# Kernel optimization log

Measured on AMD Instinct MI355X. Metric: run time of the kernel, lower is better.

Reference implementation:

```python
import jax, jax.numpy as jnp
import numpy as np
from jax import lax

D = 768          # embed_dim
H = 12           # n_heads
DEPTH = 2
T = 6            # n_timepoints
PS = 7           # patch_size
IMG = (56, 49, 49)
GRID = (8, 7, 7)
NPATCH = 392     # prod(GRID), must be even for the sinusoidal PE
SEQ = T * NPATCH # 2352 space-time tokens
MLP_H = 3072     # int(768 * 4.0)
B = 2
RRELU_MLP = 0.4        # eval-mode RReLU(0.1, 0.7) slope
RRELU_HEAD = 11.0/48.0 # eval-mode RReLU(1/8, 1/3) slope


def _ln(x, g, b, eps=1e-6):
    m = x.mean(-1, keepdims=True)
    v = ((x - m) ** 2).mean(-1, keepdims=True)
    return (x - m) / jnp.sqrt(v + eps) * g + b


def _pos_enc(t, d):
    pos = np.arange(t, dtype=np.float32)[:, None]
    div = 1.0 / 10000.0 ** (np.arange(0, d, 2, dtype=np.float32) / d)
    pe = np.zeros((t, d), np.float32)
    pe[:, 0::2] = np.sin(pos * div)
    pe[:, 1::2] = np.cos(pos * div)
    return jnp.asarray(pe)


def _convT_dw(x, w, bias, stride, dilation):
    # depthwise ConvTranspose3d(C, C, k, stride, dilation, groups=C); w: (C,1,k,k,k)
    C = x.shape[1]
    k = w.shape[-1]
    wf = jnp.flip(w, axis=(2, 3, 4))
    pad = (k - 1) * dilation
    y = lax.conv_general_dilated(
        x, wf, window_strides=(1, 1, 1), padding=[(pad, pad)] * 3,
        lhs_dilation=(stride,) * 3, rhs_dilation=(dilation,) * 3,
        dimension_numbers=('NCDHW', 'OIDHW', 'NCDHW'), feature_group_count=C)
    return y + bias[None, :, None, None, None]


def _nearest(x, size):
    # torch F.interpolate(mode='nearest'): src = floor(dst * in/out)
    for ax, s in zip((2, 3, 4), size):
        idx = (jnp.arange(s) * (x.shape[ax] / s)).astype(jnp.int32)
        x = jnp.take(x, idx, axis=ax)
    return x


def setup_inputs() -> dict:
    key = jax.random.key(0)
    ks = iter(jax.random.split(key, 64))
    def rn(shape, s=0.02):
        return jax.random.normal(next(ks), shape, jnp.float32) * s
    inp = {}
    inp['x'] = jax.random.normal(next(ks), (B, 1, T) + IMG, jnp.float32)
    inp['pconv_w'] = rn((D, 1, PS, PS, PS)); inp['pconv_b'] = rn((D,))
    inp['pos_embed'] = rn((1, SEQ, D))
    inp['ln1_g'] = jnp.ones((DEPTH, D)); inp['ln1_b'] = jnp.zeros((DEPTH, D))
    inp['qkv_w'] = rn((DEPTH, 3 * D, D)); inp['qkv_b'] = rn((DEPTH, 3 * D))
    inp['proj_w'] = rn((DEPTH, D, D)); inp['proj_b'] = rn((DEPTH, D))
    inp['ln2_g'] = jnp.ones((DEPTH, D)); inp['ln2_b'] = jnp.zeros((DEPTH, D))
    inp['fc1_w'] = rn((DEPTH, MLP_H, D)); inp['fc1_b'] = rn((DEPTH, MLP_H))
    inp['fc2_w'] = rn((DEPTH, D, MLP_H)); inp['fc2_b'] = rn((DEPTH, D))
    inp['normf_g'] = jnp.ones((D,)); inp['normf_b'] = jnp.zeros((D,))
    inp['dfc_w'] = rn((1, D)); inp['dfc_b'] = rn((1,))
    inp['up1_w'] = rn((T, 1, 7, 7, 7)); inp['up1_b'] = rn((T,))
    inp['up2_w'] = rn((T, 1, 5, 5, 5)); inp['up2_b'] = rn((T,))
    inp['up3_w'] = rn((T, 1, 9, 9, 9)); inp['up3_b'] = rn((T,))
    inp['hconv_w'] = rn((T, 1, 1, 1, 1)); inp['hconv_b'] = rn((T,))
    return inp


def reference(x, pconv_w, pconv_b, pos_embed, ln1_g, ln1_b, qkv_w, qkv_b,
              proj_w, proj_b, ln2_g, ln2_b, fc1_w, fc1_b, fc2_w, fc2_b,
              normf_g, normf_b, dfc_w, dfc_b, up1_w, up1_b, up2_w, up2_b,
              up3_w, up3_b, hconv_w, hconv_b):
    b = x.shape[0]
    hd = D // H
    scale = hd ** -0.5
    # fold time into batch, patch-embed each 3D frame
    xt = x.transpose(0, 2, 1, 3, 4, 5).reshape(b * T, 1, *IMG)
    y = lax.conv_general_dilated(
        xt, pconv_w, (PS, PS, PS), 'VALID',
        dimension_numbers=('NCDHW', 'OIDHW', 'NCDHW'))
    y = y + pconv_b[None, :, None, None, None]
    tok = y.reshape(b * T, D, NPATCH).transpose(0, 2, 1).reshape(b, SEQ, D)
    tok = tok + pos_embed
    for i in range(DEPTH):
        h = _ln(tok, ln1_g[i], ln1_b[i])
        qkv = (h @ qkv_w[i].T + qkv_b[i]).reshape(b, SEQ, 3, H, hd)
        qkv = qkv.transpose(2, 0, 3, 1, 4)  # (3,b,H,SEQ,hd)
        q, k, v = qkv[0], qkv[1], qkv[2]
        attn = jax.nn.softmax(jnp.einsum('bhnd,bhmd->bhnm', q, k) * scale, axis=-1)
        o = jnp.einsum('bhnm,bhmd->bhnd', attn, v)
        o = o.transpose(0, 2, 1, 3).reshape(b, SEQ, D)
        tok = tok + (o @ proj_w[i].T + proj_b[i])
        h = _ln(tok, ln2_g[i], ln2_b[i])
        h = h @ fc1_w[i].T + fc1_b[i]
        h = jnp.where(h >= 0, h, RRELU_MLP * h)
        tok = tok + (h @ fc2_w[i].T + fc2_b[i])
    tok = _ln(tok, normf_g, normf_b)
    z = tok.reshape(b, T, NPATCH, D)
    # --- DecoderHead ---
    z = (z @ dfc_w.T + dfc_b)[..., 0]           # (b,T,NPATCH)
    z = z - z.mean(axis=1, keepdims=True)       # subtract time mean
    z = z + _pos_enc(T, NPATCH)
    z = z.reshape(b, T, *GRID)                  # (b,T,8,7,7)
    z = _convT_dw(z, up1_w, up1_b, 1, 1)        # -> (b,T,14,13,13)
    z = _convT_dw(z, up2_w, up2_b, 2, 1)        # -> (b,T,31,29,29)
    z = _convT_dw(z, up3_w, up3_b, 1, 2)        # -> (b,T,47,45,45)
    z = _nearest(z, IMG)                        # -> (b,T,56,49,49)
    z = z * hconv_w[:, 0, 0, 0, 0][None, :, None, None, None] \
        + hconv_b[None, :, None, None, None]
    z = jnp.where(z >= 0, z, RRELU_HEAD * z)
    return z[:, None].transpose(0, 1, 3, 4, 5, 2)  # (b,1,56,49,49,T)
```

## Files before the change

### kernel.cpp

```cpp
#include <hip/hip_runtime.h>


#define AS1 __attribute__((address_space(1)))
#define AS3 __attribute__((address_space(3)))

using bf16 = __bf16;
typedef __bf16 bf16x8 __attribute__((ext_vector_type(8)));
typedef float  f32x4  __attribute__((ext_vector_type(4)));

#define CDIV(a, b) (((a) + (b) - 1) / (b))

__device__ __forceinline__ void gll16(const void* g, void* l) {
  __builtin_amdgcn_global_load_lds((AS1 void*)(void*)g, (AS3 void*)l, 16, 0, 0);
}

template <int SH>
__device__ __forceinline__ float rorf(float x) {
  int i = __builtin_amdgcn_update_dpp(0, __builtin_bit_cast(int, x),
                                      0x120 + SH, 0xF, 0xF, false);
  return __builtin_bit_cast(float, i);
}
__device__ __forceinline__ float rowsum16(float v) {
  v += rorf<1>(v); v += rorf<2>(v); v += rorf<4>(v); v += rorf<8>(v);
  return v;
}

__global__ __launch_bounds__(256) void gemm_bt(
    const bf16* __restrict__ A, const bf16* __restrict__ B,
    float* Cf, bf16* Cb, const float* __restrict__ bias,
    const float* addp, int addmod, int rrelu,
    int M, int N, int K, int lda, int ldb, int ldc,
    long long sA, long long sB, long long sC, int ksplit,
    bf16* __restrict__ Qo, bf16* __restrict__ Ko, bf16* __restrict__ Vo) {
  __shared__ __align__(16) bf16 As[2][128 * 32];
  __shared__ __align__(16) bf16 Bs[2][128 * 32];
  const int tid  = threadIdx.x;
  const int lane = tid & 63;
  const int wave = tid >> 6;
  const int wm = wave & 1;
  const int wn = wave >> 1;
  const int q  = lane >> 4;
  const int r  = lane & 15;

  const int nwg = gridDim.x * gridDim.y;
  int flat = blockIdx.y * gridDim.x + blockIdx.x;
  {
    const int qq = nwg >> 3, rr = nwg & 7;
    const int xcd = flat & 7, lid = flat >> 3;
    flat = (xcd < rr ? xcd * (qq + 1) : rr * (qq + 1) + (xcd - rr) * qq) + lid;
  }
  const int tm0 = (flat % gridDim.x) * 128;
  const int tn0 = (flat / gridDim.x) * 128;
  const int z   = blockIdx.z;

  const bf16* Ab = A + (ksplit > 1 ? 0 : (size_t)z * (size_t)sA);
  const bf16* Bb = B + (ksplit > 1 ? 0 : (size_t)z * (size_t)sB);
  int kb = 0, ke = K;
  if (ksplit > 1) {
    const int kc = ((K / ksplit + 31) / 32) * 32;
    kb = z * kc;
    ke = min(kb + kc, K);
  }

  const int arow0 = min(tm0 + (tid >> 2), M - 1);
  const int arow1 = min(tm0 + (tid >> 2) + 64, M - 1);
  const int brow0 = min(tn0 + (tid >> 2), N - 1);
  const int brow1 = min(tn0 + (tid >> 2) + 64, N - 1);
  const int kcol  = (tid & 3) * 8;
  const bf16* ap0 = Ab + (size_t)arow0 * lda + kcol;
  const bf16* ap1 = Ab + (size_t)arow1 * lda + kcol;
  const bf16* bp0 = Bb + (size_t)brow0 * ldb + kcol;
  const bf16* bp1 = Bb + (size_t)brow1 * ldb + kcol;

  f32x4 acc[4][4];
#pragma unroll
  for (int mi = 0; mi < 4; ++mi)
#pragma unroll
    for (int ni = 0; ni < 4; ++ni) acc[mi][ni] = (f32x4){0.f, 0.f, 0.f, 0.f};

  auto stage = [&](int buf, int k0) {
    bf16* as = &As[buf][wave * 512];
    bf16* bs = &Bs[buf][wave * 512];
    gll16(ap0 + k0, as);
    gll16(ap1 + k0, as + 2048);
    gll16(bp0 + k0, bs);
    gll16(bp1 + k0, bs + 2048);
  };

  stage(0, kb);
  int t = 0;
  for (int k0 = kb; k0 < ke; k0 += 32, ++t) {
    const int cur = t & 1;
    __syncthreads();
    if (k0 + 32 < ke) stage(cur ^ 1, k0 + 32);
    bf16x8 af[4], bfr[4];
#pragma unroll
    for (int mi = 0; mi < 4; ++mi)
      af[mi] = *(const bf16x8*)&As[cur][(wm * 64 + mi * 16 + r) * 32 + q * 8];
#pragma unroll
    for (int ni = 0; ni < 4; ++ni)
      bfr[ni] = *(const bf16x8*)&Bs[cur][(wn * 64 + ni * 16 + r) * 32 + q * 8];
#pragma unroll
    for (int mi = 0; mi < 4; ++mi)
#pragma unroll
      for (int ni = 0; ni < 4; ++ni)
        acc[mi][ni] = __builtin_amdgcn_mfma_f32_16x16x32_bf16(
            af[mi], bfr[ni], acc[mi][ni], 0, 0, 0);
  }

  float* cf = Cf ? Cf + (ksplit > 1 ? 0 : (size_t)z * (size_t)sC) : nullptr;
  bf16*  cb = Cb ? Cb + (ksplit > 1 ? 0 : (size_t)z * (size_t)sC) : nullptr;
#pragma unroll
  for (int mi = 0; mi < 4; ++mi) {
    const int row0 = tm0 + wm * 64 + mi * 16 + q * 4;
#pragma unroll
    for (int ni = 0; ni < 4; ++ni) {
      const int col = tn0 + wn * 64 + ni * 16 + r;
      if (col >= N) continue;
      const float bv = bias ? bias[col] : 0.f;
#pragma unroll
      for (int reg = 0; reg < 4; ++reg) {
        const int rr = row0 + reg;
        if (rr >= M) continue;
        if (Qo) {
          const float v = acc[mi][ni][reg] + bv;
          const int which = col / 768;
          const int hh = (col % 768) >> 6;
          const int dd = col & 63;
          const int bb2 = rr / 2352;
          const int ss = rr - bb2 * 2352;
          const int inst = bb2 * 12 + hh;
          if (which == 0)
            Qo[((size_t)inst * 2432 + ss) * 64 + dd] = (bf16)v;
          else if (which == 1)
            Ko[((size_t)inst * 2368 + ss) * 64 + dd] = (bf16)(v * 0.18033688f);
          else
            Vo[((size_t)inst * 64 + dd) * 2368 + ss] = (bf16)v;
        } else if (ksplit > 1) {
          float v = acc[mi][ni][reg];
          if (z == 0) {
            v += bv;
            if (addp) v += addp[(size_t)(rr % addmod) * ldc + col];
          }
          atomicAdd(&cf[(size_t)rr * ldc + col], v);
        } else {
          float v = acc[mi][ni][reg] + bv;
          if (addp) v += addp[(size_t)(rr % addmod) * ldc + col];
          if (rrelu) v = (v >= 0.f) ? v : 0.4f * v;
          if (cf) cf[(size_t)rr * ldc + col] = v;
          else    cb[(size_t)rr * ldc + col] = (bf16)v;
        }
      }
    }
  }
}

__global__ __launch_bounds__(256) void flash_attn_split(
    const bf16* __restrict__ Qg, const bf16* __restrict__ Kg,
    const bf16* __restrict__ Vt, float* __restrict__ Opart,
    float* __restrict__ Lpart) {
  __shared__ __align__(16) bf16 Kl[64 * 64];
  __shared__ __align__(16) bf16 Vl[64 * 64];
  __shared__ __align__(16) bf16 Plds[4][2][16 * 72];
  const int tid  = threadIdx.x;
  const int lane = tid & 63;
  const int wave = tid >> 6;
  const int q = lane >> 4, r = lane & 15;
  const int inst = blockIdx.y;
  const int z = blockIdx.z;
  const int rt_raw = blockIdx.x * 4 + wave;
  const int rt = min(rt_raw, 73);
  const int row0 = rt * 32;
  const int ch0 = (z * 37) >> 1;
  const int ch1 = ((z + 1) * 37) >> 1;
  const bf16* Qi = Qg + (size_t)inst * 2432 * 64;
  const bf16* Ki = Kg + (size_t)inst * 2368 * 64;
  const bf16* Vi = Vt + (size_t)inst * 64 * 2368;

  bf16x8 qf[2][2];
#pragma unroll
  for (int t = 0; t < 2; ++t) {
    qf[t][0] = *(const bf16x8*)&Qi[(size_t)(row0 + t * 16 + r) * 64 + q * 8];
    qf[t][1] = *(const bf16x8*)&Qi[(size_t)(row0 + t * 16 + r) * 64 + 32 + q * 8];
  }

  f32x4 O[2][4];
  float l[2][4];
#pragma unroll
  for (int t = 0; t < 2; ++t)
#pragma unroll
    for (int i = 0; i < 4; ++i) {
      O[t][i] = (f32x4){0.f, 0.f, 0.f, 0.f};
      l[t][i] = 0.f;
    }

  const int srow = tid >> 3;
  const int suc  = tid & 7;
  const int gu   = (suc ^ (srow & 7)) * 8;
  bf16* const kd0 = &Kl[srow * 64 + suc * 8];
  bf16* const kd1 = &Kl[(srow + 32) * 64 + suc * 8];
  bf16* const vd0 = &Vl[srow * 64 + suc * 8];
  bf16* const vd1 = &Vl[(srow + 32) * 64 + suc * 8];
  const int swz = (r & 7);

  bf16x8 kr0, kr1, vr0, vr1;
  auto loadKV = [&](int ch) {
    const size_t col0 = (size_t)ch * 64;
    kr0 = *(const bf16x8*)&Ki[(col0 + srow) * 64 + gu];
    kr1 = *(const bf16x8*)&Ki[(col0 + srow + 32) * 64 + gu];
    vr0 = *(const bf16x8*)&Vi[(size_t)srow * 2368 + col0 + gu];
    vr1 = *(const bf16x8*)&Vi[(size_t)(srow + 32) * 2368 + col0 + gu];
  };

  loadKV(ch0);
  for (int ch = ch0; ch < ch1; ++ch) {
    asm volatile("s_waitcnt lgkmcnt(0)" ::: "memory");
    __builtin_amdgcn_sched_barrier(0);
    __builtin_amdgcn_s_barrier();
    asm volatile("" ::: "memory");
    *(bf16x8*)kd0 = kr0;
    *(bf16x8*)kd1 = kr1;
    *(bf16x8*)vd0 = vr0;
    *(bf16x8*)vd1 = vr1;
    if (ch + 1 < ch1) loadKV(ch + 1);
    asm volatile("s_waitcnt lgkmcnt(0)" ::: "memory");
    __builtin_amdgcn_sched_barrier(0);
    __builtin_amdgcn_s_barrier();
    asm volatile("" ::: "memory");

    bf16x8 kf0[4], kf1[4], vf0[4], vf1[4];
#pragma unroll
    for (int ct = 0; ct < 4; ++ct) {
      const int krow = ct * 16 + r;
      kf0[ct] = *(const bf16x8*)&Kl[krow * 64 + ((q ^ swz) * 8)];
      kf1[ct] = *(const bf16x8*)&Kl[krow * 64 + (((q + 4) ^ swz) * 8)];
      vf0[ct] = *(const bf16x8*)&Vl[krow * 64 + ((q ^ swz) * 8)];
      vf1[ct] = *(const bf16x8*)&Vl[krow * 64 + (((q + 4) ^ swz) * 8)];
    }

    f32x4 s[2][4];
#pragma unroll
    for (int ct = 0; ct < 4; ++ct) {
#pragma unroll
      for (int t = 0; t < 2; ++t) {
        f32x4 a = (f32x4){0.f, 0.f, 0.f, 0.f};
        a = __builtin_amdgcn_mfma_f32_16x16x32_bf16(qf[t][0], kf0[ct], a, 0, 0, 0);
        a = __builtin_amdgcn_mfma_f32_16x16x32_bf16(qf[t][1], kf1[ct], a, 0, 0, 0);
        s[t][ct] = a;
      }
    }
    if (ch == 36) {
      s[0][3] = (f32x4){-1e30f, -1e30f, -1e30f, -1e30f};
      s[1][3] = (f32x4){-1e30f, -1e30f, -1e30f, -1e30f};
    }
#pragma unroll
    for (int t = 0; t < 2; ++t) {
      float csum[4] = {0.f, 0.f, 0.f, 0.f};
#pragma unroll
      for (int ct = 0; ct < 4; ++ct)
#pragma unroll
        for (int reg = 0; reg < 4; ++reg) {
          float p = exp2f(s[t][ct][reg]);
          s[t][ct][reg] = p;
          csum[reg] += p;
        }
#pragma unroll
      for (int reg = 0; reg < 4; ++reg)
        l[t][reg] += rowsum16(csum[reg]);
      bf16* Pw = Plds[wave][t];
#pragma unroll
      for (int ct = 0; ct < 4; ++ct)
#pragma unroll
        for (int reg = 0; reg < 4; ++reg)
          Pw[(q * 4 + reg) * 72 + ct * 16 + r] = (bf16)s[t][ct][reg];
    }
#pragma unroll
    for (int t = 0; t < 2; ++t) {
      const bf16* Pw = Plds[wave][t];
      const bf16x8 pf0 = *(const bf16x8*)&Pw[r * 72 + q * 8];
      const bf16x8 pf1 = *(const bf16x8*)&Pw[r * 72 + 32 + q * 8];
#pragma unroll
      for (int ot = 0; ot < 4; ++ot) {
        O[t][ot] = __builtin_amdgcn_mfma_f32_16x16x32_bf16(pf0, vf0[ot], O[t][ot], 0, 0, 0);
        O[t][ot] = __builtin_amdgcn_mfma_f32_16x16x32_bf16(pf1, vf1[ot], O[t][ot], 0, 0, 0);
      }
    }
  }
  if (rt_raw < 74) {
#pragma unroll
    for (int t = 0; t < 2; ++t) {
      const int p = (z * 24 + inst) * 152 + rt * 2 + t;
      float* Op = Opart + (size_t)p * 1024;
#pragma unroll
      for (int ot = 0; ot < 4; ++ot)
#pragma unroll
        for (int reg = 0; reg < 4; ++reg)
          Op[(q * 4 + reg) * 64 + ot * 16 + r] = O[t][ot][reg];
      if (r == 0) {
#pragma unroll
        for (int reg = 0; reg < 4; ++reg)
          Lpart[(size_t)p * 16 + q * 4 + reg] = l[t][reg];
      }
    }
  }
}

__global__ __launch_bounds__(256) void attn_combine(
    const float* __restrict__ Opart, const float* __restrict__ Lpart,
    bf16* __restrict__ Og) {
  const int tile = blockIdx.x;
  const int inst = blockIdx.y;
  const int bb = inst / 12, hh = inst % 12;
  const int pb = inst * 152 + tile;
#pragma unroll
  for (int i = 0; i < 4; ++i) {
    const int e = threadIdx.x + 256 * i;
    const int row = e >> 6, col = e & 63;
    const float lsum = Lpart[(size_t)pb * 16 + row] +
                       Lpart[(size_t)(3648 + pb) * 16 + row];
    const float osum = Opart[(size_t)pb * 1024 + e] +
                       Opart[(size_t)(3648 + pb) * 1024 + e];
    Og[(size_t)(bb * 2352 + tile * 16 + row) * 768 + hh * 64 + col] =
        (bf16)(osum / lsum);
  }
}


__global__ void zero_pads(bf16* __restrict__ Q, bf16* __restrict__ Kb,
                          bf16* __restrict__ VT) {
  int i = blockIdx.x * 256 + threadIdx.x;
  if (i < 122880) {
    int inst = i / 5120, rem = i % 5120;
    Q[((size_t)inst * 2432 + 2352 + rem / 64) * 64 + (rem & 63)] = (bf16)0.f;
  }
  if (i < 24576) {
    int inst = i / 1024, rem = i % 1024;
    Kb[((size_t)inst * 2368 + 2352 + rem / 64) * 64 + (rem & 63)] = (bf16)0.f;
  }
  if (i < 24576) {
    int inst = i / 1024, rem = i % 1024;
    VT[((size_t)inst * 64 + rem / 16) * 2368 + 2352 + (rem & 15)] = (bf16)0.f;
  }
}

__global__ void cvt_bf16(const float* __restrict__ x, bf16* __restrict__ y, int n) {
  int i = blockIdx.x * 256 + threadIdx.x;
  if (i < n) y[i] = (bf16)x[i];
}

__global__ void prep_pconv(const float* __restrict__ w, bf16* __restrict__ y) {
  int i = blockIdx.x * 256 + threadIdx.x;
  if (i >= 768 * 352) return;
  int d = i / 352, j = i % 352;
  y[i] = (bf16)(j < 343 ? w[d * 343 + j] : 0.f);
}

__global__ void im2col(const float* __restrict__ x, bf16* __restrict__ A) {
  int i = blockIdx.x * 256 + threadIdx.x;
  if (i >= 4704 * 352) return;
  int j = i % 352, tok = i / 352;
  float v = 0.f;
  if (j < 343) {
    int p = tok % 392, bt = tok / 392;
    int kx = j % 7, ky = (j / 7) % 7, kz = j / 49;
    int px = p % 7, py = (p / 7) % 7, pz = p / 49;
    int zz = pz * 7 + kz, yy = py * 7 + ky, xx = px * 7 + kx;
    v = x[(((size_t)bt * 56 + zz) * 49 + yy) * 49 + xx];
  }
  A[i] = (bf16)v;
}

template <typename OT>
__global__ __launch_bounds__(256) void ln_kernel(
    const float* __restrict__ x, const float* __restrict__ g,
    const float* __restrict__ bb, OT* __restrict__ y, int M) {
  int row = blockIdx.x * 4 + (threadIdx.x >> 6);
  int lane = threadIdx.x & 63;
  if (row >= M) return;
  const float* xr = x + (size_t)row * 768;
  float v[12], s = 0.f;
#pragma unroll
  for (int i = 0; i < 12; ++i) { v[i] = xr[lane + i * 64]; s += v[i]; }
#pragma unroll
  for (int off = 32; off; off >>= 1) s += __shfl_xor(s, off, 64);
  float mean = s * (1.f / 768.f);
  float vs = 0.f;
#pragma unroll
  for (int i = 0; i < 12; ++i) { float d = v[i] - mean; vs += d * d; }
#pragma unroll
  for (int off = 32; off; off >>= 1) vs += __shfl_xor(vs, off, 64);
  float inv = 1.f / sqrtf(vs * (1.f / 768.f) + 1e-6f);
#pragma unroll
  for (int i = 0; i < 12; ++i) {
    int j = lane + i * 64;
    y[(size_t)row * 768 + j] = (OT)((v[i] - mean) * inv * g[j] + bb[j]);
  }
}

__global__ __launch_bounds__(256) void dfc_kernel(
    const float* __restrict__ x, const float* __restrict__ w,
    const float* __restrict__ b0, float* __restrict__ z0, int M) {
  int row = blockIdx.x * 4 + (threadIdx.x >> 6);
  int lane = threadIdx.x & 63;
  if (row >= M) return;
  const float* xr = x + (size_t)row * 768;
  float s = 0.f;
#pragma unroll
  for (int i = 0; i < 12; ++i) s += xr[lane + i * 64] * w[lane + i * 64];
#pragma unroll
  for (int off = 32; off; off >>= 1) s += __shfl_xor(s, off, 64);
  if (lane == 0) z0[row] = s + b0[0];
}

__global__ void head_pe(const float* __restrict__ z0, float* __restrict__ z1) {
  int i = blockIdx.x * 256 + threadIdx.x;
  if (i >= 784) return;
  int b = i / 392, p = i % 392;
  float vals[6], m = 0.f;
#pragma unroll
  for (int t = 0; t < 6; ++t) { vals[t] = z0[(b * 6 + t) * 392 + p]; m += vals[t]; }
  m *= (1.f / 6.f);
  float e = (float)(2 * (p >> 1)) / 392.0f;
  float div = powf(10000.f, -e);
#pragma unroll
  for (int t = 0; t < 6; ++t) {
    float arg = (float)t * div;
    float pe = (p & 1) ? cosf(arg) : sinf(arg);
    z1[(b * 6 + t) * 392 + p] = vals[t] - m + pe;
  }
}

template <int ID, int IH, int IW, int PD, int PH, int PWA, int OFF, int ST>
__global__ void pad_in(const float* __restrict__ x, float* __restrict__ Xp) {
  int i = blockIdx.x * 256 + threadIdx.x;
  constexpr int total = 12 * PD * PH * PWA;
  if (i >= total) return;
  int px = i % PWA, t1 = i / PWA;
  int py = t1 % PH, t2 = t1 / PH;
  int pz = t2 % PD, c = t2 / PD;
  float v = 0.f;
  int tz = pz - OFF, ty = py - OFF, tx = px - OFF;
  if (tz >= 0 && ty >= 0 && tx >= 0 &&
      (ST == 1 || (((tz | ty | tx) & 1) == 0))) {
    int iz = tz / ST, iy = ty / ST, ix = tx / ST;
    if (iz < ID && iy < IH && ix < IW)
      v = x[((size_t)(c * ID + iz) * IH + iy) * IW + ix];
  }
  Xp[i] = v;
}

template <int PD, int PH, int PWA, int OD, int OH, int OW, int K, int DIL>
__global__ __launch_bounds__(256) void convt4(
    const float* __restrict__ Xp, const float* __restrict__ w,
    const float* __restrict__ bias, float* __restrict__ y) {
  constexpr int P0  = (K - 1) * DIL;
  constexpr int QX  = (OW + 3) / 4;
  constexpr int NLD = (P0 + 4 + 3) / 4;
  int idx = blockIdx.x * 256 + threadIdx.x;
  if (idx >= OD * OH * QX) return;
  int c = blockIdx.y;
  int qx = idx % QX; int t1 = idx / QX;
  int oy = t1 % OH;  int oz = t1 / OH;
  int ox0 = qx * 4;
  const float* xc = Xp + (size_t)c * (PD * PH * PWA);
  const float* wc = w + (c % 6) * (K * K * K);
  const float bv = bias[c % 6];
  float a0 = bv, a1 = bv, a2 = bv, a3 = bv;
  for (int kz = 0; kz < K; ++kz) {
    const int bz = oz + P0 - kz * DIL;
#pragma unroll
    for (int ky = 0; ky < K; ++ky) {
      const int by = oy + P0 - ky * DIL;
      const float* base = xc + ((size_t)bz * PH + by) * PWA + ox0;
      float buf[NLD * 4];
#pragma unroll
      for (int i = 0; i < NLD; ++i)
        *(f32x4*)&buf[i * 4] = *(const f32x4*)(base + i * 4);
      const float* wr = wc + (kz * K + ky) * K;
#pragma unroll
      for (int kx = 0; kx < K; ++kx) {
        const float wv = wr[kx];
        const int j = P0 - kx * DIL;
        a0 += wv * buf[j + 0];
        a1 += wv * buf[j + 1];
        a2 += wv * buf[j + 2];
        a3 += wv * buf[j + 3];
      }
    }
  }
  float* yp = y + (size_t)c * (OD * OH * OW) + ((size_t)oz * OH + oy) * OW + ox0;
  yp[0] = a0;
  if (ox0 + 1 < OW) yp[1] = a1;
  if (ox0 + 2 < OW) yp[2] = a2;
  if (ox0 + 3 < OW) yp[3] = a3;
}

__global__ void head_final(const float* __restrict__ z4, const float* __restrict__ hw,
                           const float* __restrict__ hb, float* __restrict__ out) {
  int idx = blockIdx.x * 256 + threadIdx.x;
  if (idx >= 1613472) return;
  int t = idx % 6, rdx = idx / 6;
  int xx = rdx % 49; rdx /= 49;
  int yy = rdx % 49; rdx /= 49;
  int zz = rdx % 56; int b = rdx / 56;
  const float rz = (float)(47.0 / 56.0), ry = (float)(45.0 / 49.0);
  int iz = (int)((float)zz * rz);
  int iy = (int)((float)yy * ry);
  int ix = (int)((float)xx * ry);
  float v = z4[(((size_t)(b * 6 + t) * 47 + iz) * 45 + iy) * 45 + ix];
  v = v * hw[t] + hb[t];
  v = (v >= 0.f) ? v : (11.0f / 48.0f) * v;
  out[idx] = v;
}


static inline void launch_gemm(hipStream_t s, const bf16* A, const bf16* B,
                               float* Cf, bf16* Cb, const float* bias,
                               const float* addp, int addmod, int rrelu,
                               int M, int N, int K, int lda, int ldb, int ldc,
                               long long sA, long long sB, long long sC,
                               int nz, int ksplit = 1,
                               bf16* Qo = nullptr, bf16* Ko = nullptr,
                               bf16* Vo = nullptr) {
  dim3 g(CDIV(M, 128), CDIV(N, 128), ksplit > 1 ? ksplit : nz);
  gemm_bt<<<g, 256, 0, s>>>(A, B, Cf, Cb, bias, addp, addmod, rrelu,
                            M, N, K, lda, ldb, ldc, sA, sB, sC, ksplit,
                            Qo, Ko, Vo);
}

extern "C" void kernel_launch(void* const* d_in, const int* in_sizes, int n_in,
                              void* d_out, int out_size, void* d_ws, size_t ws_size,
                              hipStream_t stream) {
  (void)in_sizes; (void)n_in; (void)out_size; (void)ws_size;
  const float* x       = (const float*)d_in[0];
  const float* pconv_w = (const float*)d_in[1];
  const float* pconv_b = (const float*)d_in[2];
  const float* pos_emb = (const float*)d_in[3];
  const float* ln1_g   = (const float*)d_in[4];
  const float* ln1_b   = (const float*)d_in[5];
  const float* qkv_wf  = (const float*)d_in[6];
  const float* qkv_b   = (const float*)d_in[7];
  const float* proj_wf = (const float*)d_in[8];
  const float* proj_b  = (const float*)d_in[9];
  const float* ln2_g   = (const float*)d_in[10];
  const float* ln2_b   = (const float*)d_in[11];
  const float* fc1_wf  = (const float*)d_in[12];
  const float* fc1_b   = (const float*)d_in[13];
  const float* fc2_wf  = (const float*)d_in[14];
  const float* fc2_b   = (const float*)d_in[15];
  const float* normf_g = (const float*)d_in[16];
  const float* normf_b = (const float*)d_in[17];
  const float* dfc_w   = (const float*)d_in[18];
  const float* dfc_b   = (const float*)d_in[19];
  const float* up1_w   = (const float*)d_in[20];
  const float* up1_b   = (const float*)d_in[21];
  const float* up2_w   = (const float*)d_in[22];
  const float* up2_b   = (const float*)d_in[23];
  const float* up3_w   = (const float*)d_in[24];
  const float* up3_b   = (const float*)d_in[25];
  const float* hconv_w = (const float*)d_in[26];
  const float* hconv_b = (const float*)d_in[27];
  float* out = (float*)d_out;

  char* ws = (char*)d_ws;
  size_t off = 0;
  auto alloc = [&](size_t bytes) -> void* {
    void* p = ws + off;
    off += (bytes + 255) & ~(size_t)255;
    return p;
  };
  float* tok   = (float*)alloc(4704UL * 768 * 4);
  bf16* lnout  = (bf16*)alloc(4704UL * 768 * 2);
  bf16* Qb     = (bf16*)alloc(24UL * 2432 * 64 * 2);
  bf16* Kb     = (bf16*)alloc(24UL * 2368 * 64 * 2);
  bf16* VT     = (bf16*)alloc(24UL * 64 * 2368 * 2);
  bf16* attnb  = (bf16*)alloc(4704UL * 768 * 2);
  bf16* hb     = (bf16*)alloc(4704UL * 3072 * 2);
  bf16* Apatch = (bf16*)alloc(4704UL * 352 * 2);
  bf16* Wq     = (bf16*)alloc(2UL * 2304 * 768 * 2);
  bf16* Wp     = (bf16*)alloc(2UL * 768 * 768 * 2);
  bf16* W1     = (bf16*)alloc(2UL * 3072 * 768 * 2);
  bf16* W2     = (bf16*)alloc(2UL * 768 * 3072 * 2);
  bf16* Wpc    = (bf16*)alloc(768UL * 352 * 2);
  float* Opart = (float*)alloc(2UL * 24 * 152 * 1024 * 4);
  float* Lpart = (float*)alloc(2UL * 24 * 152 * 16 * 4);
  float* z0    = (float*)alloc(4704UL * 4);
  float* z1    = (float*)alloc(4704UL * 4);
  float* z2    = (float*)alloc(12UL * 14 * 13 * 13 * 4);
  float* z3    = (float*)alloc(12UL * 31 * 29 * 29 * 4);
  float* z4    = (float*)alloc(12UL * 47 * 45 * 45 * 4);
  float* p1    = (float*)alloc(12UL * 20 * 19 * 24 * 4);
  float* p2    = (float*)alloc(12UL * 35 * 33 * 36 * 4);
  float* p3    = (float*)alloc(12UL * 63 * 61 * 64 * 4);
  float* lnf   = (float*)alloc(4704UL * 768 * 4);

  cvt_bf16<<<CDIV(3538944, 256), 256, 0, stream>>>(qkv_wf, Wq, 3538944);
  cvt_bf16<<<CDIV(1179648, 256), 256, 0, stream>>>(proj_wf, Wp, 1179648);
  cvt_bf16<<<CDIV(4718592, 256), 256, 0, stream>>>(fc1_wf, W1, 4718592);
  cvt_bf16<<<CDIV(4718592, 256), 256, 0, stream>>>(fc2_wf, W2, 4718592);
  prep_pconv<<<CDIV(768 * 352, 256), 256, 0, stream>>>(pconv_w, Wpc);
  zero_pads<<<CDIV(122880, 256), 256, 0, stream>>>(Qb, Kb, VT);

  im2col<<<CDIV(4704 * 352, 256), 256, 0, stream>>>(x, Apatch);
  launch_gemm(stream, Apatch, Wpc, tok, nullptr, pconv_b, pos_emb, 2352, 0,
              4704, 768, 352, 352, 352, 768, 0, 0, 0, 1);

  for (int i = 0; i < 2; ++i) {
    ln_kernel<bf16><<<1176, 256, 0, stream>>>(tok, ln1_g + i * 768, ln1_b + i * 768, lnout, 4704);
    launch_gemm(stream, lnout, Wq + (size_t)i * 2304 * 768, nullptr, nullptr,
                qkv_b + i * 2304, nullptr, 1, 0,
                4704, 2304, 768, 768, 768, 2304, 0, 0, 0, 1, 1, Qb, Kb, VT);
    flash_attn_split<<<dim3(19, 24, 2), 256, 0, stream>>>(Qb, Kb, VT, Opart, Lpart);
    attn_combine<<<dim3(147, 24), 256, 0, stream>>>(Opart, Lpart, attnb);
    launch_gemm(stream, attnb, Wp + (size_t)i * 768 * 768, tok, nullptr,
                proj_b + i * 768, nullptr, 1, 0,
                4704, 768, 768, 768, 768, 768, 0, 0, 0, 1, 4);
    ln_kernel<bf16><<<1176, 256, 0, stream>>>(tok, ln2_g + i * 768, ln2_b + i * 768, lnout, 4704);
    launch_gemm(stream, lnout, W1 + (size_t)i * 3072 * 768, nullptr, hb,
                fc1_b + i * 3072, nullptr, 1, 1,
                4704, 3072, 768, 768, 768, 3072, 0, 0, 0, 1);
    launch_gemm(stream, hb, W2 + (size_t)i * 768 * 3072, tok, nullptr,
                fc2_b + i * 768, nullptr, 1, 0,
                4704, 768, 3072, 3072, 3072, 768, 0, 0, 0, 1, 4);
  }

  ln_kernel<float><<<1176, 256, 0, stream>>>(tok, normf_g, normf_b, lnf, 4704);
  dfc_kernel<<<1176, 256, 0, stream>>>(lnf, dfc_w, dfc_b, z0, 4704);
  head_pe<<<4, 256, 0, stream>>>(z0, z1);

  pad_in<8, 7, 7, 20, 19, 24, 6, 1>
      <<<CDIV(12 * 20 * 19 * 24, 256), 256, 0, stream>>>(z1, p1);
  convt4<20, 19, 24, 14, 13, 13, 7, 1>
      <<<dim3(CDIV(14 * 13 * 4, 256), 12), 256, 0, stream>>>(p1, up1_w, up1_b, z2);
  pad_in<14, 13, 13, 35, 33, 36, 4, 2>
      <<<CDIV(12 * 35 * 33 * 36, 256), 256, 0, stream>>>(z2, p2);
  convt4<35, 33, 36, 31, 29, 29, 5, 1>
      <<<dim3(CDIV(31 * 29 * 8, 256), 12), 256, 0, stream>>>(p2, up2_w, up2_b, z3);
  pad_in<31, 29, 29, 63, 61, 64, 16, 1>
      <<<CDIV(12 * 63 * 61 * 64, 256), 256, 0, stream>>>(z3, p3);
  convt4<63, 61, 64, 47, 45, 45, 9, 2>
      <<<dim3(CDIV(47 * 45 * 12, 256), 12), 256, 0, stream>>>(p3, up3_w, up3_b, z4);

  head_final<<<CDIV(1613472, 256), 256, 0, stream>>>(z4, hconv_w, hconv_b, out);
}
```

Baseline: 1.062 ms.

## Register-staged GEMM prefetch pipeline and defer attention row-sum reduction

The GEMM kernel stops using direct global-to-LDS async loads. Each tile is now loaded into registers two iterations ahead and written to the alternate LDS buffer after the MFMA block, with one explicit barrier per iteration. This is meant to overlap global latency with compute and drop the per-iteration syncthreads. Separately, the attention kernel keeps per-lane partial row sums and runs the cross-lane DPP reduction once at the end instead of every chunk, which cuts shuffle work in the inner loop. The register staging raises VGPR pressure, and the single barrier relies on the LDS write ordering being correct.

```diff
diff --git a/kernel.cpp b/kernel.cpp
--- a/kernel.cpp
+++ b/kernel.cpp
@@ -9,10 +9,6 @@
 typedef float  f32x4  __attribute__((ext_vector_type(4)));
 
 #define CDIV(a, b) (((a) + (b) - 1) / (b))
-
-__device__ __forceinline__ void gll16(const void* g, void* l) {
-  __builtin_amdgcn_global_load_lds((AS1 void*)(void*)g, (AS3 void*)l, 16, 0, 0);
-}
 
 template <int SH>
 __device__ __forceinline__ float rorf(float x) {
@@ -61,6 +57,7 @@
     kb = z * kc;
     ke = min(kb + kc, K);
   }
+  const int nt = (ke - kb + 31) >> 5;
 
   const int arow0 = min(tm0 + (tid >> 2), M - 1);
   const int arow1 = min(tm0 + (tid >> 2) + 64, M - 1);
@@ -78,21 +75,31 @@
 #pragma unroll
     for (int ni = 0; ni < 4; ++ni) acc[mi][ni] = (f32x4){0.f, 0.f, 0.f, 0.f};
 
-  auto stage = [&](int buf, int k0) {
-    bf16* as = &As[buf][wave * 512];
-    bf16* bs = &Bs[buf][wave * 512];
-    gll16(ap0 + k0, as);
-    gll16(ap1 + k0, as + 2048);
-    gll16(bp0 + k0, bs);
-    gll16(bp1 + k0, bs + 2048);
+  bf16x8 rA0, rA1, rB0, rB1;
+  auto loadT = [&](int t) {
+    const int k0 = kb + (t << 5);
+    rA0 = *(const bf16x8*)(ap0 + k0);
+    rA1 = *(const bf16x8*)(ap1 + k0);
+    rB0 = *(const bf16x8*)(bp0 + k0);
+    rB1 = *(const bf16x8*)(bp1 + k0);
   };
-
-  stage(0, kb);
-  int t = 0;
-  for (int k0 = kb; k0 < ke; k0 += 32, ++t) {
+  auto writeT = [&](int buf) {
+    *(bf16x8*)&As[buf][tid * 8]        = rA0;
+    *(bf16x8*)&As[buf][2048 + tid * 8] = rA1;
+    *(bf16x8*)&Bs[buf][tid * 8]        = rB0;
+    *(bf16x8*)&Bs[buf][2048 + tid * 8] = rB1;
+  };
+
+  loadT(0);
+  writeT(0);
+  if (nt > 1) loadT(1);
+
+  for (int t = 0; t < nt; ++t) {
     const int cur = t & 1;
-    __syncthreads();
-    if (k0 + 32 < ke) stage(cur ^ 1, k0 + 32);
+    asm volatile("s_waitcnt lgkmcnt(0)" ::: "memory");
+    __builtin_amdgcn_sched_barrier(0);
+    __builtin_amdgcn_s_barrier();
+    asm volatile("" ::: "memory");
     bf16x8 af[4], bfr[4];
 #pragma unroll
     for (int mi = 0; mi < 4; ++mi)
@@ -106,6 +113,11 @@
       for (int ni = 0; ni < 4; ++ni)
         acc[mi][ni] = __builtin_amdgcn_mfma_f32_16x16x32_bf16(
             af[mi], bfr[ni], acc[mi][ni], 0, 0, 0);
+    __builtin_amdgcn_sched_barrier(0);
+    if (t + 1 < nt) {
+      writeT(cur ^ 1);
+      if (t + 2 < nt) loadT(t + 2);
+    }
   }
 
   float* cf = Cf ? Cf + (ksplit > 1 ? 0 : (size_t)z * (size_t)sC) : nullptr;
@@ -266,7 +278,7 @@
         }
 #pragma unroll
       for (int reg = 0; reg < 4; ++reg)
-        l[t][reg] += rowsum16(csum[reg]);
+        l[t][reg] += csum[reg];
       bf16* Pw = Plds[wave][t];
 #pragma unroll
       for (int ct = 0; ct < 4; ++ct)
@@ -286,6 +298,11 @@
       }
     }
   }
+#pragma unroll
+  for (int t = 0; t < 2; ++t)
+#pragma unroll
+    for (int i = 0; i < 4; ++i) l[t][i] = rowsum16(l[t][i]);
+
   if (rt_raw < 74) {
 #pragma unroll
     for (int t = 0; t < 2; ++t) {
```

Measured after the change: 1.038 ms. 2.3% less time.
